# Kernel tuning notes

Measured on AMD Instinct MI355X. Metric: run time of the kernel, lower is better.

## Reference

```python
import jax, jax.numpy as jnp
import numpy as np

NUM_NODES = 80000
NUM_EDGES = 1280000
NUM_GRAPHS = 512
IN_DIM = 64
HID = 64
NUM_CLASSES = 10


def setup_inputs() -> dict:
    key = jax.random.key(0)
    ks = jax.random.split(key, 16)
    x = jax.random.normal(ks[0], (NUM_NODES, IN_DIM), dtype=jnp.float32)
    edge_index = jax.random.randint(ks[1], (2, NUM_EDGES), 0, NUM_NODES, dtype=jnp.int64)
    batch = jnp.sort(jax.random.randint(ks[2], (NUM_NODES,), 0, NUM_GRAPHS, dtype=jnp.int64))

    def glorot(k, shape):
        fan_in, fan_out = shape[1], shape[0]
        lim = jnp.sqrt(6.0 / (fan_in + fan_out))
        return jax.random.uniform(k, shape, dtype=jnp.float32, minval=-lim, maxval=lim)

    inp = {
        "x": x,
        "edge_index": edge_index,
        "batch": batch,
        # GraphConv layer 1: lin_rel (with bias) applied to aggregated neighbors, lin_root (no bias)
        "w_rel1": glorot(ks[3], (HID, IN_DIM)),
        "b_rel1": jnp.zeros((HID,), dtype=jnp.float32),
        "w_root1": glorot(ks[4], (HID, IN_DIM)),
        # layer 2
        "w_rel2": glorot(ks[5], (HID, HID)),
        "b_rel2": jnp.zeros((HID,), dtype=jnp.float32),
        "w_root2": glorot(ks[6], (HID, HID)),
        # layer 3
        "w_rel3": glorot(ks[7], (HID, HID)),
        "b_rel3": jnp.zeros((HID,), dtype=jnp.float32),
        "w_root3": glorot(ks[8], (HID, HID)),
        # final linear head
        "w_lin": glorot(ks[9], (NUM_CLASSES, HID)),
        "b_lin": jnp.zeros((NUM_CLASSES,), dtype=jnp.float32),
    }
    return inp


def _graph_conv(x, src, dst, w_rel, b_rel, w_root):
    # PyG GraphConv with aggr='add': out_i = W_rel @ (sum_{j in N(i)} x_j) + b_rel + W_root @ x_i
    agg = jax.ops.segment_sum(x[src], dst, num_segments=NUM_NODES)  # [N, d_in]
    return agg @ w_rel.T + b_rel + x @ w_root.T


def reference(x, edge_index, batch,
              w_rel1, b_rel1, w_root1,
              w_rel2, b_rel2, w_root2,
              w_rel3, b_rel3, w_root3,
              w_lin, b_lin):
    src, dst = edge_index[0], edge_index[1]
    h = jax.nn.relu(_graph_conv(x, src, dst, w_rel1, b_rel1, w_root1))
    h = jax.nn.relu(_graph_conv(h, src, dst, w_rel2, b_rel2, w_root2))
    h = _graph_conv(h, src, dst, w_rel3, b_rel3, w_root3)
    # global_mean_pool over graph ids
    sums = jax.ops.segment_sum(h, batch, num_segments=NUM_GRAPHS)          # [G, HID]
    counts = jax.ops.segment_sum(jnp.ones((h.shape[0],), h.dtype), batch, num_segments=NUM_GRAPHS)
    pooled = sums / jnp.maximum(counts, 1.0)[:, None]
    # dropout p=0.5 is identity at inference (training=False)
    return pooled @ w_lin.T + b_lin  # [G, NUM_CLASSES]
```

## Files before the change

### kernel.cpp

```cpp
#include <hip/hip_runtime.h>

#define N_NODES  80000
#define N_EDGES  1280000
#define N_GRAPHS 512
#define DIM      64
#define NCLS     10

#define ETILE    8192
#define NTILE    157
#define NCB      157
#define CBPAD    160

typedef short short8f __attribute__((ext_vector_type(8)));
typedef float float4f __attribute__((ext_vector_type(4)));

static __device__ __forceinline__ unsigned short f2bf(float f) {
    unsigned u = __float_as_uint(f);
    unsigned r = (u + 0x7FFFu + ((u >> 16) & 1u)) >> 16;
    return (unsigned short)r;
}
static __device__ __forceinline__ float bf_lo(unsigned v) { return __uint_as_float(v << 16); }
static __device__ __forceinline__ float bf_hi(unsigned v) { return __uint_as_float(v & 0xFFFF0000u); }

__global__ __launch_bounds__(256) void k_hist(const int* __restrict__ ei,
                                              int* __restrict__ hmat) {
    __shared__ int hist[NCB];
    int tile = blockIdx.x, t = threadIdx.x;
    for (int i = t; i < NCB; i += 256) hist[i] = 0;
    __syncthreads();
    int base = tile * ETILE;
    int end = base + ETILE; if (end > N_EDGES) end = N_EDGES;
    for (int i = base + t; i < end; i += 256)
        atomicAdd(&hist[ei[N_EDGES + i] >> 9], 1);
    __syncthreads();
    for (int i = t; i < NCB; i += 256) hmat[tile * CBPAD + i] = hist[i];
}

__global__ __launch_bounds__(256) void k_scanT(const int* __restrict__ hmat,
        int* __restrict__ obase, int* __restrict__ btot) {
    __shared__ int sa[256], sb[256];
    int b = blockIdx.x, t = threadIdx.x;
    int v = (t < NTILE) ? hmat[t * CBPAD + b] : 0;
    sa[t] = v; __syncthreads();
    int* sp = sa; int* dp = sb;
    for (int off = 1; off < 256; off <<= 1) {
        dp[t] = sp[t] + ((t >= off) ? sp[t - off] : 0);
        __syncthreads();
        int* tmp = sp; sp = dp; dp = tmp;
    }
    int incl = sp[t];
    if (t < NTILE) obase[t * CBPAD + b] = incl - v;
    if (t == NTILE - 1) btot[b] = incl;
}

__global__ __launch_bounds__(256) void k_scanB(const int* __restrict__ btot,
        int* __restrict__ bucketbase, int* __restrict__ rowptr) {
    __shared__ int sa[256], sb[256];
    int t = threadIdx.x;
    int v = (t < NCB) ? btot[t] : 0;
    sa[t] = v; __syncthreads();
    int* sp = sa; int* dp = sb;
    for (int off = 1; off < 256; off <<= 1) {
        dp[t] = sp[t] + ((t >= off) ? sp[t - off] : 0);
        __syncthreads();
        int* tmp = sp; sp = dp; dp = tmp;
    }
    int incl = sp[t];
    if (t < NCB) bucketbase[t] = incl - v;
    if (t == 0) { bucketbase[NCB] = N_EDGES; rowptr[N_NODES] = N_EDGES; }
}

__global__ __launch_bounds__(256) void k_scatter(const int* __restrict__ ei,
        const int* __restrict__ obase, const int* __restrict__ bucketbase,
        int* __restrict__ ebuf) {
    __shared__ int cur[NCB];
    int tile = blockIdx.x, t = threadIdx.x;
    for (int i = t; i < NCB; i += 256)
        cur[i] = bucketbase[i] + obase[tile * CBPAD + i];
    __syncthreads();
    int base = tile * ETILE;
    int end = base + ETILE; if (end > N_EDGES) end = N_EDGES;
    for (int i = base + t; i < end; i += 256) {
        int s = ei[i], d = ei[N_EDGES + i];
        int p = atomicAdd(&cur[d >> 9], 1);
        ebuf[p] = s | ((d & 511) << 17);
    }
}

__global__ __launch_bounds__(256) void k_csr(const int* __restrict__ ebuf,
        const int* __restrict__ bucketbase, int* __restrict__ rowptr,
        int* __restrict__ col) {
    __shared__ int cnt[512];
    __shared__ int sa[512], sb[512];
    __shared__ int cur[512];
    int b = blockIdx.x, t = threadIdx.x;
    int s = bucketbase[b], e = bucketbase[b + 1];
    cnt[t] = 0; cnt[t + 256] = 0;
    __syncthreads();
    for (int i = s + t; i < e; i += 256) atomicAdd(&cnt[ebuf[i] >> 17], 1);
    __syncthreads();
    sa[t] = cnt[t]; sa[t + 256] = cnt[t + 256];
    __syncthreads();
    int* sp = sa; int* dp = sb;
    for (int off = 1; off < 512; off <<= 1) {
        int i1 = t + 256;
        int v0 = sp[t]  + ((t  >= off) ? sp[t  - off] : 0);
        int v1 = sp[i1] + ((i1 >= off) ? sp[i1 - off] : 0);
        __syncthreads();
        dp[t] = v0; dp[i1] = v1;
        __syncthreads();
        int* tmp = sp; sp = dp; dp = tmp;
    }
    int node0 = b * 512;
    int base0 = s + sp[t] - cnt[t];
    int base1 = s + sp[t + 256] - cnt[t + 256];
    cur[t] = base0; cur[t + 256] = base1;
    if (node0 + t < N_NODES)       rowptr[node0 + t] = base0;
    if (node0 + t + 256 < N_NODES) rowptr[node0 + t + 256] = base1;
    __syncthreads();
    for (int i = s + t; i < e; i += 256) {
        int pk = ebuf[i];
        int p = atomicAdd(&cur[pk >> 17], 1);
        col[p] = pk & 0x1FFFF;
    }
}

__global__ __launch_bounds__(256) void k_prep2(const float* __restrict__ x,
        const float* __restrict__ wr1, const float* __restrict__ wo1,
        const float* __restrict__ wr2, const float* __restrict__ wo2,
        const float* __restrict__ wr3, const float* __restrict__ wo3,
        unsigned short* __restrict__ xb, unsigned short* __restrict__ wf) {
    int bid = blockIdx.x, t = threadIdx.x;
    if (bid < 5000) {
        int i = bid * 256 + t;
        float4 v = ((const float4*)x)[i];
        ushort4 o;
        o.x = f2bf(v.x); o.y = f2bf(v.y); o.z = f2bf(v.z); o.w = f2bf(v.w);
        ((ushort4*)xb)[i] = o;
    } else {
        int idx = (bid - 5000) * 256 + t;
        int j = idx & 7, lane = (idx >> 3) & 63;
        int ks = (idx >> 9) & 3, nt = (idx >> 11) & 3, l = idx >> 13;
        int k = ks * 32 + ((lane >> 4) & 3) * 8 + j;
        int n = nt * 16 + (lane & 15);
        const float* wr = (l == 0) ? wr1 : (l == 1) ? wr2 : wr3;
        const float* wo = (l == 0) ? wo1 : (l == 1) ? wo2 : wo3;
        float val = (k < 64) ? wr[n * 64 + k] : wo[n * 64 + (k - 64)];
        wf[idx] = f2bf(val);
    }
}

__global__ __launch_bounds__(256) void k_gather_bf(const unsigned short* __restrict__ Xbf,
        const int* __restrict__ rowptr, const int* __restrict__ col,
        unsigned short* __restrict__ agg) {
    const unsigned* Xu = (const unsigned*)Xbf;
    int t = threadIdx.x, w = t >> 6, lane = t & 63;
    int g = lane >> 5, c = lane & 31;
    int node = blockIdx.x * 8 + w * 2 + g;
    int start = rowptr[node], end = rowptr[node + 1];
    float alo = 0.f, ahi = 0.f;
    int e = start;
    for (; e + 16 <= end; e += 16) {
        unsigned v[16];
#pragma unroll
        for (int j = 0; j < 16; ++j)
            v[j] = Xu[(size_t)col[e + j] * 32 + c];
#pragma unroll
        for (int j = 0; j < 16; ++j) { alo += bf_lo(v[j]); ahi += bf_hi(v[j]); }
    }
    for (; e + 4 <= end; e += 4) {
        unsigned v0 = Xu[(size_t)col[e]     * 32 + c];
        unsigned v1 = Xu[(size_t)col[e + 1] * 32 + c];
        unsigned v2 = Xu[(size_t)col[e + 2] * 32 + c];
        unsigned v3 = Xu[(size_t)col[e + 3] * 32 + c];
        alo += (bf_lo(v0) + bf_lo(v1)) + (bf_lo(v2) + bf_lo(v3));
        ahi += (bf_hi(v0) + bf_hi(v1)) + (bf_hi(v2) + bf_hi(v3));
    }
    for (; e < end; ++e) {
        unsigned v = Xu[(size_t)col[e] * 32 + c];
        alo += bf_lo(v); ahi += bf_hi(v);
    }
    unsigned o = (unsigned)f2bf(alo) | ((unsigned)f2bf(ahi) << 16);
    ((unsigned*)agg)[(size_t)node * 32 + c] = o;
}

__global__ __launch_bounds__(256) void k_linear_mfma(
        const unsigned short* __restrict__ aggb, const unsigned short* __restrict__ xb,
        const unsigned short* __restrict__ wf, const float* __restrict__ bias,
        unsigned short* __restrict__ out, int relu) {
    int t = threadIdx.x, w = t >> 6, lane = t & 63;
    int quad = lane >> 4, l15 = lane & 15;
    int mbase = blockIdx.x * 64 + w * 16;
    size_t arow = (size_t)(mbase + l15) * 64;
    short8f a0 = *(const short8f*)(aggb + arow + quad * 8);
    short8f a1 = *(const short8f*)(aggb + arow + 32 + quad * 8);
    short8f a2 = *(const short8f*)(xb   + arow + quad * 8);
    short8f a3 = *(const short8f*)(xb   + arow + 32 + quad * 8);
    int orow = mbase + quad * 4;
#pragma unroll
    for (int nt = 0; nt < 4; ++nt) {
        const unsigned short* wp = wf + ((size_t)(nt * 4) * 64 + lane) * 8;
        short8f b0 = *(const short8f*)(wp);
        short8f b1 = *(const short8f*)(wp + 64 * 8);
        short8f b2 = *(const short8f*)(wp + 128 * 8);
        short8f b3 = *(const short8f*)(wp + 192 * 8);
        float4f acc = {0.f, 0.f, 0.f, 0.f};
        acc = __builtin_amdgcn_mfma_f32_16x16x32_bf16(a0, b0, acc, 0, 0, 0);
        acc = __builtin_amdgcn_mfma_f32_16x16x32_bf16(a1, b1, acc, 0, 0, 0);
        acc = __builtin_amdgcn_mfma_f32_16x16x32_bf16(a2, b2, acc, 0, 0, 0);
        acc = __builtin_amdgcn_mfma_f32_16x16x32_bf16(a3, b3, acc, 0, 0, 0);
        float bi = bias[nt * 16 + l15];
#pragma unroll
        for (int r = 0; r < 4; ++r) {
            float v = acc[r] + bi;
            if (relu) v = fmaxf(v, 0.f);
            out[(size_t)(orow + r) * 64 + nt * 16 + l15] = f2bf(v);
        }
    }
}

static __device__ __forceinline__ int lowerb(const int* a, int n, int key) {
    int lo = 0, hi = n;
    while (lo < hi) { int mid = (lo + hi) >> 1; if (a[mid] < key) lo = mid + 1; else hi = mid; }
    return lo;
}

__global__ __launch_bounds__(256) void k_poolhead(const unsigned short* __restrict__ h,
        const int* __restrict__ batch, const float* __restrict__ wlin,
        const float* __restrict__ blin, float* __restrict__ out) {
    __shared__ float sp[8][64];
    int gph = blockIdx.x;
    int t = threadIdx.x, sub = t >> 5, c = t & 31;
    int start = lowerb(batch, N_NODES, gph);
    int end   = lowerb(batch, N_NODES, gph + 1);
    const unsigned* hu = (const unsigned*)h;
    float alo = 0.f, ahi = 0.f;
    for (int i = start + sub; i < end; i += 8) {
        unsigned v = hu[(size_t)i * 32 + c];
        alo += bf_lo(v); ahi += bf_hi(v);
    }
    sp[sub][2 * c] = alo; sp[sub][2 * c + 1] = ahi;
    __syncthreads();
    if (t < 64) {
        float v = 0.f;
#pragma unroll
        for (int s = 0; s < 8; ++s) v += sp[s][t];
        int cnt = end - start;
        v /= (float)((cnt > 0) ? cnt : 1);
        float myout = 0.f;
        for (int cls = 0; cls < NCLS; ++cls) {
            float vv = v * wlin[cls * 64 + t];
            for (int off = 32; off > 0; off >>= 1) vv += __shfl_xor(vv, off);
            if (t == cls) myout = vv + blin[cls];
        }
        if (t < NCLS) out[gph * NCLS + t] = myout;
    }
}

extern "C" void kernel_launch(void* const* d_in, const int* in_sizes, int n_in,
                              void* d_out, int out_size, void* d_ws, size_t ws_size,
                              hipStream_t stream) {
    const float* x     = (const float*)d_in[0];
    const int*   ei    = (const int*)d_in[1];
    const int*   batch = (const int*)d_in[2];
    const float* wr1 = (const float*)d_in[3];
    const float* b1  = (const float*)d_in[4];
    const float* wo1 = (const float*)d_in[5];
    const float* wr2 = (const float*)d_in[6];
    const float* b2  = (const float*)d_in[7];
    const float* wo2 = (const float*)d_in[8];
    const float* wr3 = (const float*)d_in[9];
    const float* b3  = (const float*)d_in[10];
    const float* wo3 = (const float*)d_in[11];
    const float* wlin = (const float*)d_in[12];
    const float* blin = (const float*)d_in[13];
    float* out = (float*)d_out;

    char* p = (char*)d_ws;
    auto alloc = [&](size_t bytes) { char* r = p; p += (bytes + 255) & ~(size_t)255; return r; };
    int*   rowptr  = (int*)alloc((N_NODES + 1) * sizeof(int));
    int*   hmat    = (int*)alloc((size_t)NTILE * CBPAD * sizeof(int));
    int*   obase   = (int*)alloc((size_t)NTILE * CBPAD * sizeof(int));
    int*   btot    = (int*)alloc(CBPAD * sizeof(int));
    int*   bucketbase = (int*)alloc((NCB + 1) * sizeof(int));
    int*   ebuf    = (int*)alloc((size_t)N_EDGES * sizeof(int));
    int*   col     = (int*)alloc((size_t)N_EDGES * sizeof(int));
    unsigned short* wf  = (unsigned short*)alloc(3 * 8192 * sizeof(unsigned short));
    unsigned short* xbf = (unsigned short*)alloc((size_t)N_NODES * 64 * 2);
    unsigned short* agg = (unsigned short*)alloc((size_t)N_NODES * 64 * 2);
    unsigned short* hA  = (unsigned short*)alloc((size_t)N_NODES * 64 * 2);
    unsigned short* hB  = (unsigned short*)alloc((size_t)N_NODES * 64 * 2);

    k_hist   <<<NTILE, 256, 0, stream>>>(ei, hmat);
    k_scanT  <<<NCB,   256, 0, stream>>>(hmat, obase, btot);
    k_scanB  <<<1,     256, 0, stream>>>(btot, bucketbase, rowptr);
    k_scatter<<<NTILE, 256, 0, stream>>>(ei, obase, bucketbase, ebuf);
    k_csr    <<<NCB,   256, 0, stream>>>(ebuf, bucketbase, rowptr, col);
    k_prep2  <<<5096,  256, 0, stream>>>(x, wr1, wo1, wr2, wo2, wr3, wo3, xbf, wf);

    k_gather_bf  <<<N_NODES / 8,  256, 0, stream>>>(xbf, rowptr, col, agg);
    k_linear_mfma<<<N_NODES / 64, 256, 0, stream>>>(agg, xbf, wf,         b1, hA, 1);
    k_gather_bf  <<<N_NODES / 8,  256, 0, stream>>>(hA, rowptr, col, agg);
    k_linear_mfma<<<N_NODES / 64, 256, 0, stream>>>(agg, hA, wf + 8192,   b2, hB, 1);
    k_gather_bf  <<<N_NODES / 8,  256, 0, stream>>>(hB, rowptr, col, agg);
    k_linear_mfma<<<N_NODES / 64, 256, 0, stream>>>(agg, hB, wf + 16384,  b3, hA, 0);

    k_poolhead<<<N_GRAPHS, 256, 0, stream>>>(hA, batch, wlin, blin, out);
}
```

Measured before the change: 277.4 us.

## Fold linear third layer into pooling by pooling before the final transform

The third GraphConv layer has no activation, so its linear maps commute with mean pooling. Instead of gathering neighbours for every node and running a third MFMA linear pass, each graph block sums neighbour features over the CSR edge range of its nodes plus its own node features. A small head kernel then applies the layer-3 weights, bias and the classifier to the per-graph means. This removes a full-node gather pass and a linear pass, at the cost of a per-graph loop that may be load-imbalanced. It relies on nodes being sorted by graph so that each graph's edges form one contiguous CSR range.

```diff
diff --git a/kernel.cpp b/kernel.cpp
--- a/kernel.cpp
+++ b/kernel.cpp
@@ -128,7 +128,6 @@
 __global__ __launch_bounds__(256) void k_prep2(const float* __restrict__ x,
         const float* __restrict__ wr1, const float* __restrict__ wo1,
         const float* __restrict__ wr2, const float* __restrict__ wo2,
-        const float* __restrict__ wr3, const float* __restrict__ wo3,
         unsigned short* __restrict__ xb, unsigned short* __restrict__ wf) {
     int bid = blockIdx.x, t = threadIdx.x;
     if (bid < 5000) {
@@ -143,8 +142,8 @@
         int ks = (idx >> 9) & 3, nt = (idx >> 11) & 3, l = idx >> 13;
         int k = ks * 32 + ((lane >> 4) & 3) * 8 + j;
         int n = nt * 16 + (lane & 15);
-        const float* wr = (l == 0) ? wr1 : (l == 1) ? wr2 : wr3;
-        const float* wo = (l == 0) ? wo1 : (l == 1) ? wo2 : wo3;
+        const float* wr = (l == 0) ? wr1 : wr2;
+        const float* wo = (l == 0) ? wo1 : wo2;
         float val = (k < 64) ? wr[n * 64 + k] : wo[n * 64 + (k - 64)];
         wf[idx] = f2bf(val);
     }
@@ -225,36 +224,79 @@
     return lo;
 }
 
-__global__ __launch_bounds__(256) void k_poolhead(const unsigned short* __restrict__ h,
-        const int* __restrict__ batch, const float* __restrict__ wlin,
-        const float* __restrict__ blin, float* __restrict__ out) {
-    __shared__ float sp[8][64];
-    int gph = blockIdx.x;
-    int t = threadIdx.x, sub = t >> 5, c = t & 31;
-    int start = lowerb(batch, N_NODES, gph);
-    int end   = lowerb(batch, N_NODES, gph + 1);
-    const unsigned* hu = (const unsigned*)h;
+__global__ __launch_bounds__(256) void k_gsum(const unsigned short* __restrict__ h2,
+        const int* __restrict__ rowptr, const int* __restrict__ col,
+        const int* __restrict__ batch, float* __restrict__ S) {
+    __shared__ float red1[8][64];
+    __shared__ float red2[8][64];
+    const unsigned* Xu = (const unsigned*)h2;
+    int g = blockIdx.x, t = threadIdx.x;
+    int hw = t >> 5, c = t & 31;
+    int ns = lowerb(batch, N_NODES, g);
+    int ne = lowerb(batch, N_NODES, g + 1);
+    int es = rowptr[ns], ee = rowptr[ne];
     float alo = 0.f, ahi = 0.f;
-    for (int i = start + sub; i < end; i += 8) {
-        unsigned v = hu[(size_t)i * 32 + c];
+    int nfull = (ee - es) >> 7;
+    int e0 = es + hw * 16;
+    for (int b = 0; b < nfull; ++b, e0 += 128) {
+        unsigned v[16];
+#pragma unroll
+        for (int j = 0; j < 16; ++j)
+            v[j] = Xu[(size_t)col[e0 + j] * 32 + c];
+#pragma unroll
+        for (int j = 0; j < 16; ++j) { alo += bf_lo(v[j]); ahi += bf_hi(v[j]); }
+    }
+    for (int e = es + nfull * 128 + hw; e < ee; e += 8) {
+        unsigned v = Xu[(size_t)col[e] * 32 + c];
         alo += bf_lo(v); ahi += bf_hi(v);
     }
-    sp[sub][2 * c] = alo; sp[sub][2 * c + 1] = ahi;
+    float blo = 0.f, bhi = 0.f;
+    for (int i = ns + hw; i < ne; i += 8) {
+        unsigned v = Xu[(size_t)i * 32 + c];
+        blo += bf_lo(v); bhi += bf_hi(v);
+    }
+    red1[hw][2 * c] = alo; red1[hw][2 * c + 1] = ahi;
+    red2[hw][2 * c] = blo; red2[hw][2 * c + 1] = bhi;
     __syncthreads();
     if (t < 64) {
         float v = 0.f;
 #pragma unroll
-        for (int s = 0; s < 8; ++s) v += sp[s][t];
-        int cnt = end - start;
-        v /= (float)((cnt > 0) ? cnt : 1);
-        float myout = 0.f;
-        for (int cls = 0; cls < NCLS; ++cls) {
-            float vv = v * wlin[cls * 64 + t];
-            for (int off = 32; off > 0; off >>= 1) vv += __shfl_xor(vv, off);
-            if (t == cls) myout = vv + blin[cls];
-        }
-        if (t < NCLS) out[gph * NCLS + t] = myout;
-    }
+        for (int s = 0; s < 8; ++s) v += red1[s][t];
+        S[g * 128 + t] = v;
+    } else if (t < 128) {
+        float v = 0.f;
+#pragma unroll
+        for (int s = 0; s < 8; ++s) v += red2[s][t - 64];
+        S[g * 128 + 64 + (t - 64)] = v;
+    }
+}
+
+__global__ __launch_bounds__(64) void k_head2(const float* __restrict__ S,
+        const int* __restrict__ batch,
+        const float* __restrict__ wr3, const float* __restrict__ wo3,
+        const float* __restrict__ b3,
+        const float* __restrict__ wlin, const float* __restrict__ blin,
+        float* __restrict__ out) {
+    __shared__ float s1[64], s2[64], pl[64];
+    int g = blockIdx.x, t = threadIdx.x;
+    int ns = lowerb(batch, N_NODES, g);
+    int ne = lowerb(batch, N_NODES, g + 1);
+    float inv = 1.f / (float)((ne > ns) ? (ne - ns) : 1);
+    s1[t] = S[g * 128 + t] * inv;
+    s2[t] = S[g * 128 + 64 + t] * inv;
+    __syncthreads();
+    float acc = b3[t];
+    for (int k = 0; k < 64; ++k)
+        acc += s1[k] * wr3[t * 64 + k] + s2[k] * wo3[t * 64 + k];
+    pl[t] = acc;
+    __syncthreads();
+    float myout = 0.f;
+    for (int cls = 0; cls < NCLS; ++cls) {
+        float vv = pl[t] * wlin[cls * 64 + t];
+        for (int off = 32; off > 0; off >>= 1) vv += __shfl_xor(vv, off);
+        if (t == cls) myout = vv + blin[cls];
+    }
+    if (t < NCLS) out[g * NCLS + t] = myout;
 }
 
 extern "C" void kernel_launch(void* const* d_in, const int* in_sizes, int n_in,
@@ -285,25 +327,24 @@
     int*   bucketbase = (int*)alloc((NCB + 1) * sizeof(int));
     int*   ebuf    = (int*)alloc((size_t)N_EDGES * sizeof(int));
     int*   col     = (int*)alloc((size_t)N_EDGES * sizeof(int));
-    unsigned short* wf  = (unsigned short*)alloc(3 * 8192 * sizeof(unsigned short));
+    unsigned short* wf  = (unsigned short*)alloc(2 * 8192 * sizeof(unsigned short));
     unsigned short* xbf = (unsigned short*)alloc((size_t)N_NODES * 64 * 2);
     unsigned short* agg = (unsigned short*)alloc((size_t)N_NODES * 64 * 2);
     unsigned short* hA  = (unsigned short*)alloc((size_t)N_NODES * 64 * 2);
     unsigned short* hB  = (unsigned short*)alloc((size_t)N_NODES * 64 * 2);
+    float* S       = (float*)alloc((size_t)N_GRAPHS * 128 * sizeof(float));
 
     k_hist   <<<NTILE, 256, 0, stream>>>(ei, hmat);
     k_scanT  <<<NCB,   256, 0, stream>>>(hmat, obase, btot);
     k_scanB  <<<1,     256, 0, stream>>>(btot, bucketbase, rowptr);
     k_scatter<<<NTILE, 256, 0, stream>>>(ei, obase, bucketbase, ebuf);
     k_csr    <<<NCB,   256, 0, stream>>>(ebuf, bucketbase, rowptr, col);
-    k_prep2  <<<5096,  256, 0, stream>>>(x, wr1, wo1, wr2, wo2, wr3, wo3, xbf, wf);
+    k_prep2  <<<5064,  256, 0, stream>>>(x, wr1, wo1, wr2, wo2, xbf, wf);
 
     k_gather_bf  <<<N_NODES / 8,  256, 0, stream>>>(xbf, rowptr, col, agg);
-    k_linear_mfma<<<N_NODES / 64, 256, 0, stream>>>(agg, xbf, wf,         b1, hA, 1);
+    k_linear_mfma<<<N_NODES / 64, 256, 0, stream>>>(agg, xbf, wf,        b1, hA, 1);
     k_gather_bf  <<<N_NODES / 8,  256, 0, stream>>>(hA, rowptr, col, agg);
-    k_linear_mfma<<<N_NODES / 64, 256, 0, stream>>>(agg, hA, wf + 8192,   b2, hB, 1);
-    k_gather_bf  <<<N_NODES / 8,  256, 0, stream>>>(hB, rowptr, col, agg);
-    k_linear_mfma<<<N_NODES / 64, 256, 0, stream>>>(agg, hB, wf + 16384,  b3, hA, 0);
-
-    k_poolhead<<<N_GRAPHS, 256, 0, stream>>>(hA, batch, wlin, blin, out);
-}
+    k_linear_mfma<<<N_NODES / 64, 256, 0, stream>>>(agg, hA, wf + 8192,  b2, hB, 1);
+    k_gsum <<<N_GRAPHS, 256, 0, stream>>>(hB, rowptr, col, batch, S);
+    k_head2<<<N_GRAPHS, 64,  0, stream>>>(S, batch, wr3, wo3, b3, wlin, blin, out);
+}
```

Measured after the change: 279.9 us. No clear change (+0.9%).
